# Kernel optimization log

Measured on AMD Instinct MI355X. Metric: run time of the kernel, lower is better.

The kernel has to match this reference:

```python
import jax, jax.numpy as jnp
import numpy as np
import math

B, T, F, H = 8, 1024, 1024, 16
D = F // H

def setup_inputs() -> dict:
    key = jax.random.key(0)
    ks = jax.random.split(key, 6)
    s = 1.0 / math.sqrt(F)
    return {
        "qkv": jax.random.normal(ks[0], (B, T, F), dtype=jnp.float32),
        "key_padding_mask": jax.random.randint(ks[1], (B, T), 0, 2).astype(bool),
        "in_proj_w": jax.random.normal(ks[2], (3 * F, F), dtype=jnp.float32) * s,
        "in_proj_b": jax.random.normal(ks[3], (3 * F,), dtype=jnp.float32) * 0.02,
        "out_proj_w": jax.random.normal(ks[4], (F, F), dtype=jnp.float32) * s,
        "out_proj_b": jax.random.normal(ks[5], (F,), dtype=jnp.float32) * 0.02,
    }

def reference(qkv, key_padding_mask, in_proj_w, in_proj_b, out_proj_w, out_proj_b):
    b, t, f = qkv.shape
    h, d = H, f // H
    norm = jnp.asarray(math.sqrt(d), dtype=qkv.dtype)
    # fused QKV projection (torch Linear: x @ W.T + b)
    x = qkv @ in_proj_w.T + in_proj_b                     # [B, T, 3F]
    q, k, v = jnp.split(x, 3, axis=-1)
    q = q.reshape(b, t, h, d).transpose(0, 2, 1, 3)       # [B, H, T, D]
    k = k.reshape(b, t, h, d).transpose(0, 2, 1, 3)
    v = v.reshape(b, t, h, d).transpose(0, 2, 1, 3)
    dot = jnp.einsum("bhqd,bhkd->bhqk", q, k) / norm      # [B, H, T, T]
    dot = jnp.where(key_padding_mask[:, None, None, :], -jnp.inf, dot)
    alpha = jax.nn.softmax(dot, axis=-1)                  # [B, H, T, T]
    att = jnp.einsum("bhqk,bhkd->bhqd", alpha, v)         # [B, H, T, D]
    att = att.transpose(0, 2, 1, 3).reshape(b, t, f)      # [B, T, F]
    out = att @ out_proj_w.T + out_proj_b
    return (out, alpha)
```

## Files before the change

kernel.cpp:

```cpp
#include <hip/hip_runtime.h>
#include <math.h>

#define B_ 8
#define T_ 1024
#define F_ 1024
#define H_ 16
#define D_ 64

typedef __bf16 bf16x8 __attribute__((ext_vector_type(8)));
typedef float f32x4 __attribute__((ext_vector_type(4)));
typedef unsigned short u16x8 __attribute__((ext_vector_type(8)));

__device__ __forceinline__ unsigned short f2bf(float f) {
    union { float f; unsigned u; } v; v.f = f;
    unsigned r = v.u + 0x7fffu + ((v.u >> 16) & 1u);
    return (unsigned short)(r >> 16);
}

__device__ __forceinline__ void gld16(const void* g, void* l) {
    __builtin_amdgcn_global_load_lds(
        (const __attribute__((address_space(1))) void*)g,
        (__attribute__((address_space(3))) void*)l, 16, 0, 0);
}

__device__ __forceinline__ int swz4(int row15) {
    return (row15 ^ (row15 >> 2)) & 3;
}

__global__ __launch_bounds__(256) void cvt_f32_bf16(
    const float* __restrict__ in, unsigned short* __restrict__ out, int n8)
{
    int i = blockIdx.x * 256 + threadIdx.x;
    if (i >= n8) return;
    const float4* p = (const float4*)in + (size_t)i * 2;
    float4 x = p[0], y = p[1];
    u16x8 o;
    o[0] = f2bf(x.x); o[1] = f2bf(x.y); o[2] = f2bf(x.z); o[3] = f2bf(x.w);
    o[4] = f2bf(y.x); o[5] = f2bf(y.y); o[6] = f2bf(y.z); o[7] = f2bf(y.w);
    ((u16x8*)out)[i] = o;
}

__global__ __launch_bounds__(256) void qkv_gemm(
    const unsigned short* __restrict__ A,
    const unsigned short* __restrict__ Bw,
    const float* __restrict__ bias,
    unsigned short* __restrict__ qb,
    unsigned short* __restrict__ kb,
    unsigned short* __restrict__ vb)
{
    __shared__ __align__(16) unsigned short As[128 * 32];
    __shared__ __align__(16) unsigned short Bs[128 * 32];
    const int K = 1024;
    int tid = threadIdx.x;
    int lane = tid & 63, wave = tid >> 6;
    int wr = wave >> 1, wc = wave & 1;
    int m0 = blockIdx.y * 128, n0 = blockIdx.x * 128;
    int col = lane & 15, quad = lane >> 4;
    int sw = swz4(col);
    int rl = lane >> 2;
    int lc = (lane & 3) ^ swz4(rl);

    f32x4 acc[4][4] = {};
    for (int kc = 0; kc < K; kc += 32) {
        __syncthreads();
        #pragma unroll
        for (int l = 0; l < 2; l++) {
            int ia = wave * 2 + l;
            gld16(A  + (size_t)(m0 + ia * 16 + rl) * K + kc + lc * 8, &As[ia * 512]);
            gld16(Bw + (size_t)(n0 + ia * 16 + rl) * K + kc + lc * 8, &Bs[ia * 512]);
        }
        __syncthreads();
        bf16x8 af[4], bg[4];
        #pragma unroll
        for (int mt = 0; mt < 4; mt++)
            af[mt] = *(const bf16x8*)&As[(wr * 64 + mt * 16 + col) * 32 + ((quad ^ sw)) * 8];
        #pragma unroll
        for (int nt = 0; nt < 4; nt++)
            bg[nt] = *(const bf16x8*)&Bs[(wc * 64 + nt * 16 + col) * 32 + ((quad ^ sw)) * 8];
        #pragma unroll
        for (int mt = 0; mt < 4; mt++)
            #pragma unroll
            for (int nt = 0; nt < 4; nt++)
                acc[mt][nt] = __builtin_amdgcn_mfma_f32_16x16x32_bf16(
                    af[mt], bg[nt], acc[mt][nt], 0, 0, 0);
    }
    int which = n0 >> 10;
    #pragma unroll
    for (int nt = 0; nt < 4; nt++) {
        int n = n0 + wc * 64 + nt * 16 + col;
        int hn = (n & 1023) >> 6, d = n & 63;
        float bn = bias[n];
        #pragma unroll
        for (int mt = 0; mt < 4; mt++) {
            #pragma unroll
            for (int r = 0; r < 4; r++) {
                int m = m0 + wr * 64 + mt * 16 + quad * 4 + r;
                int bb = m >> 10, t = m & 1023;
                unsigned short bf = f2bf(acc[mt][nt][r] + bn);
                if (which == 0)
                    qb[(size_t)((bb * H_ + hn) * T_ + t) * D_ + d] = bf;
                else if (which == 1)
                    kb[(size_t)((bb * H_ + hn) * T_ + t) * D_ + d] = bf;
                else
                    vb[(size_t)((bb * H_ + hn) * D_ + d) * T_ + t] = bf;
            }
        }
    }
}

__global__ __launch_bounds__(256) void fused_attn(
    const unsigned short* __restrict__ qb,
    const unsigned short* __restrict__ kb,
    const unsigned short* __restrict__ vb,
    const int* __restrict__ mask,
    float* __restrict__ alpha,
    unsigned short* __restrict__ attb)
{
    __shared__ __align__(16) unsigned short U[16 * 1032];
    __shared__ __align__(16) unsigned short Vs[4][2048];
    __shared__ __align__(16) unsigned short Qs[16 * 72];
    __shared__ float redmax[4][16];
    __shared__ float redsum[4][16];
    int b = blockIdx.z, h = blockIdx.y, q0 = blockIdx.x * 16;
    int tid = threadIdx.x, lane = tid & 63, wave = tid >> 6;
    int col = lane & 15, quad = lane >> 4;
    const unsigned short* qbase = qb + ((size_t)(b * H_ + h) * T_ + q0) * D_;
    const unsigned short* kbase = kb + ((size_t)(b * H_ + h) * T_) * D_;
    unsigned short* Ksw = &U[wave * 4096];

    if (tid < 128) {
        int r = tid >> 3, c = tid & 7;
        *(u16x8*)&Qs[r * 72 + c * 8] = *(const u16x8*)&qbase[r * 64 + c * 8];
    }
    int krl = lane >> 3;
    int klc = (lane & 7) ^ krl;
    int sw8 = col & 7;
    f32x4 acc[4][4] = {};
    bf16x8 aq0, aq1;
    for (int it = 0; it < 4; it++) {
        int kr0 = wave * 256 + it * 64;
        #pragma unroll
        for (int j = 0; j < 8; j++)
            gld16(kbase + (size_t)(kr0 + j * 8 + krl) * 64 + klc * 8, &Ksw[j * 512]);
        __syncthreads();
        if (it == 0) {
            aq0 = *(const bf16x8*)&Qs[col * 72 + quad * 8];
            aq1 = *(const bf16x8*)&Qs[col * 72 + 32 + quad * 8];
        }
        #pragma unroll
        for (int ct = 0; ct < 4; ct++) {
            int r = ct * 16 + col;
            const unsigned short* kp = &Ksw[r * 64];
            bf16x8 b0 = *(const bf16x8*)&kp[(quad ^ sw8) * 8];
            bf16x8 b1 = *(const bf16x8*)&kp[((4 + quad) ^ sw8) * 8];
            acc[it][ct] = __builtin_amdgcn_mfma_f32_16x16x32_bf16(aq0, b0, acc[it][ct], 0, 0, 0);
            acc[it][ct] = __builtin_amdgcn_mfma_f32_16x16x32_bf16(aq1, b1, acc[it][ct], 0, 0, 0);
        }
        __syncthreads();
    }
    const int* mrow = mask + b * T_;
    float mx[4] = {-INFINITY, -INFINITY, -INFINITY, -INFINITY};
    #pragma unroll
    for (int it = 0; it < 4; it++)
        #pragma unroll
        for (int ct = 0; ct < 4; ct++) {
            int k = wave * 256 + it * 64 + ct * 16 + col;
            bool m = mrow[k] != 0;
            #pragma unroll
            for (int r = 0; r < 4; r++) {
                float v = m ? -INFINITY : acc[it][ct][r] * 0.125f;
                acc[it][ct][r] = v;
                mx[r] = fmaxf(mx[r], v);
            }
        }
    #pragma unroll
    for (int r = 0; r < 4; r++) {
        mx[r] = fmaxf(mx[r], __shfl_xor(mx[r], 1, 64));
        mx[r] = fmaxf(mx[r], __shfl_xor(mx[r], 2, 64));
        mx[r] = fmaxf(mx[r], __shfl_xor(mx[r], 4, 64));
        mx[r] = fmaxf(mx[r], __shfl_xor(mx[r], 8, 64));
    }
    if (col == 0)
        #pragma unroll
        for (int r = 0; r < 4; r++) redmax[wave][quad * 4 + r] = mx[r];
    __syncthreads();
    float gm[4];
    #pragma unroll
    for (int r = 0; r < 4; r++) {
        int row = quad * 4 + r;
        gm[r] = fmaxf(fmaxf(redmax[0][row], redmax[1][row]),
                      fmaxf(redmax[2][row], redmax[3][row]));
    }
    float sm[4] = {0.f, 0.f, 0.f, 0.f};
    #pragma unroll
    for (int it = 0; it < 4; it++)
        #pragma unroll
        for (int ct = 0; ct < 4; ct++)
            #pragma unroll
            for (int r = 0; r < 4; r++) {
                float e = __expf(acc[it][ct][r] - gm[r]);
                acc[it][ct][r] = e;
                sm[r] += e;
            }
    #pragma unroll
    for (int r = 0; r < 4; r++) {
        sm[r] += __shfl_xor(sm[r], 1, 64);
        sm[r] += __shfl_xor(sm[r], 2, 64);
        sm[r] += __shfl_xor(sm[r], 4, 64);
        sm[r] += __shfl_xor(sm[r], 8, 64);
    }
    if (col == 0)
        #pragma unroll
        for (int r = 0; r < 4; r++) redsum[wave][quad * 4 + r] = sm[r];
    __syncthreads();
    float inv[4];
    #pragma unroll
    for (int r = 0; r < 4; r++) {
        int row = quad * 4 + r;
        inv[r] = 1.0f / (redsum[0][row] + redsum[1][row] + redsum[2][row] + redsum[3][row]);
    }
    float* abase = alpha + ((size_t)(b * H_ + h) * T_ + q0) * T_;
    #pragma unroll
    for (int it = 0; it < 4; it++)
        #pragma unroll
        for (int ct = 0; ct < 4; ct++) {
            int k = wave * 256 + it * 64 + ct * 16 + col;
            #pragma unroll
            for (int r = 0; r < 4; r++) {
                float v = acc[it][ct][r] * inv[r];
                abase[(size_t)(quad * 4 + r) * T_ + k] = v;
                U[(quad * 4 + r) * 1032 + k] = f2bf(v);
            }
        }
    __syncthreads();
    const unsigned short* vhead = vb + (size_t)(b * H_ + h) * D_ * T_;
    f32x4 oacc = {};
    for (int kc = 0; kc < T_; kc += 128) {
        asm volatile("s_waitcnt lgkmcnt(0)" ::: "memory");
        __builtin_amdgcn_sched_barrier(0);
        #pragma unroll
        for (int i = 0; i < 4; i++) {
            int r = i * 4 + quad;
            gld16(vhead + (size_t)(wave * 16 + r) * T_ + kc + (col ^ (r & 7)) * 8,
                  &Vs[wave][i * 512]);
        }
        asm volatile("s_waitcnt vmcnt(0)" ::: "memory");
        __builtin_amdgcn_sched_barrier(0);
        #pragma unroll
        for (int w = 0; w < 4; w++) {
            bf16x8 pa = *(const bf16x8*)&U[col * 1032 + kc + w * 32 + quad * 8];
            bf16x8 bv = *(const bf16x8*)&Vs[wave][col * 128 + (((w * 4 + quad) ^ (col & 7))) * 8];
            oacc = __builtin_amdgcn_mfma_f32_16x16x32_bf16(pa, bv, oacc, 0, 0, 0);
        }
    }
    #pragma unroll
    for (int r = 0; r < 4; r++) {
        int t = q0 + quad * 4 + r;
        attb[(size_t)(b * T_ + t) * F_ + h * D_ + wave * 16 + col] = f2bf(oacc[r]);
    }
}

__global__ __launch_bounds__(256) void out_gemm(
    const unsigned short* __restrict__ A,
    const unsigned short* __restrict__ Bw,
    const float* __restrict__ bias,
    float* __restrict__ out)
{
    __shared__ __align__(16) unsigned short As[128 * 32];
    __shared__ __align__(16) unsigned short Bs[128 * 32];
    const int K = 1024;
    int tid = threadIdx.x;
    int lane = tid & 63, wave = tid >> 6;
    int wr = wave >> 1, wc = wave & 1;
    int m0 = blockIdx.y * 128, n0 = blockIdx.x * 128;
    int col = lane & 15, quad = lane >> 4;
    int sw = swz4(col);
    int rl = lane >> 2;
    int lc = (lane & 3) ^ swz4(rl);
    f32x4 acc[4][4] = {};
    for (int kc = 0; kc < K; kc += 32) {
        __syncthreads();
        #pragma unroll
        for (int l = 0; l < 2; l++) {
            int ia = wave * 2 + l;
            gld16(A  + (size_t)(m0 + ia * 16 + rl) * K + kc + lc * 8, &As[ia * 512]);
            gld16(Bw + (size_t)(n0 + ia * 16 + rl) * K + kc + lc * 8, &Bs[ia * 512]);
        }
        __syncthreads();
        bf16x8 af[4], bg[4];
        #pragma unroll
        for (int mt = 0; mt < 4; mt++)
            af[mt] = *(const bf16x8*)&As[(wr * 64 + mt * 16 + col) * 32 + ((quad ^ sw)) * 8];
        #pragma unroll
        for (int nt = 0; nt < 4; nt++)
            bg[nt] = *(const bf16x8*)&Bs[(wc * 64 + nt * 16 + col) * 32 + ((quad ^ sw)) * 8];
        #pragma unroll
        for (int mt = 0; mt < 4; mt++)
            #pragma unroll
            for (int nt = 0; nt < 4; nt++)
                acc[mt][nt] = __builtin_amdgcn_mfma_f32_16x16x32_bf16(
                    af[mt], bg[nt], acc[mt][nt], 0, 0, 0);
    }
    #pragma unroll
    for (int nt = 0; nt < 4; nt++) {
        int n = n0 + wc * 64 + nt * 16 + col;
        float bn = bias[n];
        #pragma unroll
        for (int mt = 0; mt < 4; mt++) {
            #pragma unroll
            for (int r = 0; r < 4; r++) {
                int m = m0 + wr * 64 + mt * 16 + quad * 4 + r;
                out[(size_t)m * F_ + n] = acc[mt][nt][r] + bn;
            }
        }
    }
}

extern "C" void kernel_launch(void* const* d_in, const int* in_sizes, int n_in,
                              void* d_out, int out_size, void* d_ws, size_t ws_size,
                              hipStream_t stream)
{
    const float* qkv   = (const float*)d_in[0];
    const int*   mask  = (const int*)d_in[1];
    const float* in_w  = (const float*)d_in[2];
    const float* in_b  = (const float*)d_in[3];
    const float* out_w = (const float*)d_in[4];
    const float* out_b = (const float*)d_in[5];
    float* out = (float*)d_out;
    const size_t NE = (size_t)B_ * T_ * F_;
    float* alpha = out + NE;

    unsigned short* ws   = (unsigned short*)d_ws;
    unsigned short* Xb   = ws;
    unsigned short* Wib  = Xb  + NE;
    unsigned short* Wob  = Wib + 3 * F_ * F_;
    unsigned short* qb2  = Wob + (size_t)F_ * F_;
    unsigned short* kb2  = qb2 + NE;
    unsigned short* vb2  = kb2 + NE;
    unsigned short* attb = vb2 + NE;

    cvt_f32_bf16<<<dim3((int)(NE / 8 / 256)), 256, 0, stream>>>(qkv, Xb, (int)(NE / 8));
    cvt_f32_bf16<<<dim3(3 * F_ * F_ / 8 / 256), 256, 0, stream>>>(in_w, Wib, 3 * F_ * F_ / 8);
    cvt_f32_bf16<<<dim3(F_ * F_ / 8 / 256), 256, 0, stream>>>(out_w, Wob, F_ * F_ / 8);

    qkv_gemm<<<dim3(24, 64), 256, 0, stream>>>(Xb, Wib, in_b, qb2, kb2, vb2);
    fused_attn<<<dim3(64, H_, B_), 256, 0, stream>>>(qb2, kb2, vb2, mask, alpha, attb);
    out_gemm<<<dim3(8, 64), 256, 0, stream>>>(attb, Wob, out_b, out);
}
```

Baseline: 907.6 us.

## Double-buffer K and V loads per wave and drop block-wide syncs

Restructures the QK^T loop in the fused attention kernel into a per-wave double-buffered pipeline over 32-key chunks. Waits use vmcnt counters instead of __syncthreads, and Q is loaded straight from global into registers rather than staged through LDS. The V tile prefetch is issued before the softmax so it overlaps that phase, and the PV loop is double-buffered in 64-column chunks. This aims to hide global load latency and cut barrier stalls, at the cost of more in-flight loads and reliance on wave-private buffers being hazard-free across the loop.

After: 905.8 us. About the same (-0.2%).

```diff
diff --git a/kernel.cpp b/kernel.cpp
--- a/kernel.cpp
+++ b/kernel.cpp
@@ -117,8 +117,7 @@
     unsigned short* __restrict__ attb)
 {
     __shared__ __align__(16) unsigned short U[16 * 1032];
-    __shared__ __align__(16) unsigned short Vs[4][2048];
-    __shared__ __align__(16) unsigned short Qs[16 * 72];
+    __shared__ __align__(16) unsigned short Vs[4][2][1024];
     __shared__ float redmax[4][16];
     __shared__ float redsum[4][16];
     int b = blockIdx.z, h = blockIdx.y, q0 = blockIdx.x * 16;
@@ -126,45 +125,65 @@
     int col = lane & 15, quad = lane >> 4;
     const unsigned short* qbase = qb + ((size_t)(b * H_ + h) * T_ + q0) * D_;
     const unsigned short* kbase = kb + ((size_t)(b * H_ + h) * T_) * D_;
-    unsigned short* Ksw = &U[wave * 4096];
-
-    if (tid < 128) {
-        int r = tid >> 3, c = tid & 7;
-        *(u16x8*)&Qs[r * 72 + c * 8] = *(const u16x8*)&qbase[r * 64 + c * 8];
-    }
+
+    bf16x8 aq0 = *(const bf16x8*)&qbase[col * 64 + quad * 8];
+    bf16x8 aq1 = *(const bf16x8*)&qbase[col * 64 + 32 + quad * 8];
+
     int krl = lane >> 3;
     int klc = (lane & 7) ^ krl;
     int sw8 = col & 7;
-    f32x4 acc[4][4] = {};
-    bf16x8 aq0, aq1;
-    for (int it = 0; it < 4; it++) {
-        int kr0 = wave * 256 + it * 64;
-        #pragma unroll
-        for (int j = 0; j < 8; j++)
-            gld16(kbase + (size_t)(kr0 + j * 8 + krl) * 64 + klc * 8, &Ksw[j * 512]);
-        __syncthreads();
-        if (it == 0) {
-            aq0 = *(const bf16x8*)&Qs[col * 72 + quad * 8];
-            aq1 = *(const bf16x8*)&Qs[col * 72 + 32 + quad * 8];
-        }
-        #pragma unroll
-        for (int ct = 0; ct < 4; ct++) {
-            int r = ct * 16 + col;
-            const unsigned short* kp = &Ksw[r * 64];
+    unsigned short* Kb0 = &U[wave * 4096];
+    unsigned short* Kb1 = Kb0 + 2048;
+
+    #pragma unroll
+    for (int j = 0; j < 4; j++)
+        gld16(kbase + (size_t)(wave * 256 + j * 8 + krl) * 64 + klc * 8, Kb0 + j * 512);
+    #pragma unroll
+    for (int j = 0; j < 4; j++)
+        gld16(kbase + (size_t)(wave * 256 + 32 + j * 8 + krl) * 64 + klc * 8, Kb1 + j * 512);
+
+    f32x4 acc[8][2] = {};
+    #pragma unroll
+    for (int it = 0; it < 8; it++) {
+        if (it < 7) { asm volatile("s_waitcnt vmcnt(4)" ::: "memory"); }
+        else        { asm volatile("s_waitcnt vmcnt(0)" ::: "memory"); }
+        __builtin_amdgcn_sched_barrier(0);
+        const unsigned short* Kb = (it & 1) ? Kb1 : Kb0;
+        #pragma unroll
+        for (int ct = 0; ct < 2; ct++) {
+            const unsigned short* kp = Kb + (ct * 16 + col) * 64;
             bf16x8 b0 = *(const bf16x8*)&kp[(quad ^ sw8) * 8];
             bf16x8 b1 = *(const bf16x8*)&kp[((4 + quad) ^ sw8) * 8];
             acc[it][ct] = __builtin_amdgcn_mfma_f32_16x16x32_bf16(aq0, b0, acc[it][ct], 0, 0, 0);
             acc[it][ct] = __builtin_amdgcn_mfma_f32_16x16x32_bf16(aq1, b1, acc[it][ct], 0, 0, 0);
         }
-        __syncthreads();
-    }
+        __builtin_amdgcn_sched_barrier(0);
+        if (it < 6) {
+            unsigned short* Kn = (it & 1) ? Kb1 : Kb0;
+            #pragma unroll
+            for (int j = 0; j < 4; j++)
+                gld16(kbase + (size_t)(wave * 256 + (it + 2) * 32 + j * 8 + krl) * 64 + klc * 8,
+                      Kn + j * 512);
+        }
+    }
+
+    const unsigned short* vhead = vb + (size_t)(b * H_ + h) * D_ * T_;
+    int vrl = lane >> 3;
+    int vswz = (lane & 7) ^ vrl;
+    #pragma unroll
+    for (int i = 0; i < 2; i++)
+        gld16(vhead + (size_t)(wave * 16 + i * 8 + vrl) * T_ + vswz * 8, &Vs[wave][0][i * 512]);
+    #pragma unroll
+    for (int i = 0; i < 2; i++)
+        gld16(vhead + (size_t)(wave * 16 + i * 8 + vrl) * T_ + 64 + vswz * 8, &Vs[wave][1][i * 512]);
+
     const int* mrow = mask + b * T_;
     float mx[4] = {-INFINITY, -INFINITY, -INFINITY, -INFINITY};
     #pragma unroll
-    for (int it = 0; it < 4; it++)
-        #pragma unroll
-        for (int ct = 0; ct < 4; ct++) {
-            int k = wave * 256 + it * 64 + ct * 16 + col;
+    for (int it = 0; it < 8; it++)
+        #pragma unroll
+        for (int ct = 0; ct < 2; ct++) {
+            int k = wave * 256 + it * 32 + ct * 16 + col;
             bool m = mrow[k] != 0;
             #pragma unroll
             for (int r = 0; r < 4; r++) {
@@ -193,9 +212,9 @@
     }
     float sm[4] = {0.f, 0.f, 0.f, 0.f};
     #pragma unroll
-    for (int it = 0; it < 4; it++)
-        #pragma unroll
-        for (int ct = 0; ct < 4; ct++)
+    for (int it = 0; it < 8; it++)
+        #pragma unroll
+        for (int ct = 0; ct < 2; ct++)
             #pragma unroll
             for (int r = 0; r < 4; r++) {
                 float e = __expf(acc[it][ct][r] - gm[r]);
@@ -221,10 +240,10 @@
     }
     float* abase = alpha + ((size_t)(b * H_ + h) * T_ + q0) * T_;
     #pragma unroll
-    for (int it = 0; it < 4; it++)
-        #pragma unroll
-        for (int ct = 0; ct < 4; ct++) {
-            int k = wave * 256 + it * 64 + ct * 16 + col;
+    for (int it = 0; it < 8; it++)
+        #pragma unroll
+        for (int ct = 0; ct < 2; ct++) {
+            int k = wave * 256 + it * 32 + ct * 16 + col;
             #pragma unroll
             for (int r = 0; r < 4; r++) {
                 float v = acc[it][ct][r] * inv[r];
@@ -233,24 +252,25 @@
             }
         }
     __syncthreads();
-    const unsigned short* vhead = vb + (size_t)(b * H_ + h) * D_ * T_;
     f32x4 oacc = {};
-    for (int kc = 0; kc < T_; kc += 128) {
-        asm volatile("s_waitcnt lgkmcnt(0)" ::: "memory");
+    #pragma unroll
+    for (int t = 0; t < 16; t++) {
+        if (t < 15) { asm volatile("s_waitcnt vmcnt(2)" ::: "memory"); }
+        else        { asm volatile("s_waitcnt vmcnt(0)" ::: "memory"); }
         __builtin_amdgcn_sched_barrier(0);
-        #pragma unroll
-        for (int i = 0; i < 4; i++) {
-            int r = i * 4 + quad;
-            gld16(vhead + (size_t)(wave * 16 + r) * T_ + kc + (col ^ (r & 7)) * 8,
-                  &Vs[wave][i * 512]);
-        }
-        asm volatile("s_waitcnt vmcnt(0)" ::: "memory");
+        const unsigned short* Vb = Vs[wave][t & 1];
+        bf16x8 pa0 = *(const bf16x8*)&U[col * 1032 + t * 64 + quad * 8];
+        bf16x8 pa1 = *(const bf16x8*)&U[col * 1032 + t * 64 + 32 + quad * 8];
+        bf16x8 bv0 = *(const bf16x8*)&Vb[col * 64 + ((quad ^ sw8)) * 8];
+        bf16x8 bv1 = *(const bf16x8*)&Vb[col * 64 + (((quad + 4) ^ sw8)) * 8];
+        oacc = __builtin_amdgcn_mfma_f32_16x16x32_bf16(pa0, bv0, oacc, 0, 0, 0);
+        oacc = __builtin_amdgcn_mfma_f32_16x16x32_bf16(pa1, bv1, oacc, 0, 0, 0);
         __builtin_amdgcn_sched_barrier(0);
-        #pragma unroll
-        for (int w = 0; w < 4; w++) {
-            bf16x8 pa = *(const bf16x8*)&U[col * 1032 + kc + w * 32 + quad * 8];
-            bf16x8 bv = *(const bf16x8*)&Vs[wave][col * 128 + (((w * 4 + quad) ^ (col & 7))) * 8];
-            oacc = __builtin_amdgcn_mfma_f32_16x16x32_bf16(pa, bv, oacc, 0, 0, 0);
+        if (t < 14) {
+            #pragma unroll
+            for (int i = 0; i < 2; i++)
+                gld16(vhead + (size_t)(wave * 16 + i * 8 + vrl) * T_ + (t + 2) * 64 + vswz * 8,
+                      &Vs[wave][t & 1][i * 512]);
         }
     }
     #pragma unroll
```
